# Kernel optimization log

Hardware: AMD Instinct MI355X
Metric: run time of the kernel (lower is better)

Reference implementation:

```python
import jax, jax.numpy as jnp
import numpy as np

B, CIN, COUT, N, K = 8, 128, 128, 2000, 16
IN_EPS = 1e-3   # InstanceNorm2d eps in module
BN_EPS = 1e-5   # BatchNorm2d default eps


def conv1x1(x, w, b):
    # x: [B,C,H,W], w: [O,C], b: [O]
    return jnp.einsum('bchw,oc->bohw', x, w) + b[None, :, None, None]


def setup_inputs() -> dict:
    key = jax.random.key(0)
    ks = jax.random.split(key, 12)
    s = 0.05
    return {
        'x_row':   jax.random.normal(ks[0], (B, COUT, N, 1), jnp.float32),
        'x_local': jax.random.normal(ks[1], (B, CIN, N, K), jnp.float32),
        'w0': jax.random.normal(ks[2], (COUT, CIN), jnp.float32) * s,
        'b0': jax.random.normal(ks[3], (COUT,), jnp.float32) * s,
        'bn_g': jnp.ones((COUT,), jnp.float32),
        'bn_b': jnp.zeros((COUT,), jnp.float32),
        'wq': jax.random.normal(ks[4], (COUT, COUT), jnp.float32) * s,
        'bq': jax.random.normal(ks[5], (COUT,), jnp.float32) * s,
        'wk': jax.random.normal(ks[6], (COUT, COUT), jnp.float32) * s,
        'bk': jax.random.normal(ks[7], (COUT,), jnp.float32) * s,
        'wv': jax.random.normal(ks[8], (COUT, COUT), jnp.float32) * s,
        'bv': jax.random.normal(ks[9], (COUT,), jnp.float32) * s,
        'gamma1': jnp.ones((1,), jnp.float32),
    }


def reference(x_row, x_local, w0, b0, bn_g, bn_b, wq, bq, wk, bk, wv, bv, gamma1):
    # att1: Conv1x1 -> InstanceNorm2d(eps=1e-3, no affine) -> BatchNorm2d (train-mode batch stats) -> ReLU
    h = conv1x1(x_local, w0, b0)                       # [B,C,N,K]
    mu = jnp.mean(h, axis=(2, 3), keepdims=True)
    var = jnp.var(h, axis=(2, 3), keepdims=True)
    h = (h - mu) * jax.lax.rsqrt(var + IN_EPS)
    bmu = jnp.mean(h, axis=(0, 2, 3), keepdims=True)
    bvar = jnp.var(h, axis=(0, 2, 3), keepdims=True)
    h = (h - bmu) * jax.lax.rsqrt(bvar + BN_EPS)
    h = h * bn_g[None, :, None, None] + bn_b[None, :, None, None]
    h = jax.nn.relu(h)

    q = conv1x1(h, wq, bq)
    k = conv1x1(h, wk, bk)
    v = conv1x1(h, wv, bv)
    att = jax.nn.softmax(q * k, axis=3)                # softmax over neighbor axis
    out_local = jnp.sum(att * v, axis=3, keepdims=True)  # [B,C,N,1]
    return x_row + gamma1 * out_local
```

## Files before the change

kernel.cpp:

```cpp
#include <hip/hip_runtime.h>
#include <math.h>

#define NB 8
#define NC 128
#define NPOS 2000
#define NK 32000
#define IN_EPS 1e-3f
#define BN_EPS 1e-5f

typedef short bf16x8 __attribute__((ext_vector_type(8)));
typedef float f32x4 __attribute__((ext_vector_type(4)));
typedef unsigned short ushort_t;

#define XSTRIDE 136

__device__ __forceinline__ f32x4 mfma_bf16(bf16x8 a, bf16x8 b, f32x4 c) {
  return __builtin_amdgcn_mfma_f32_16x16x32_bf16(a, b, c, 0, 0, 0);
}

__device__ __forceinline__ ushort_t f2bf(float f) {
  unsigned u = __float_as_uint(f);
  return (ushort_t)((u + 0x7FFFu + ((u >> 16) & 1u)) >> 16);
}


__global__ __launch_bounds__(256) void k_prep(const float* __restrict__ w0,
    const float* __restrict__ wq, const float* __restrict__ wk,
    const float* __restrict__ wv, ushort_t* __restrict__ wb) {
  int idx = blockIdx.x * 256 + threadIdx.x;
  int m = idx >> 14;
  int e = idx & 16383;
  const float* src = (m == 0) ? w0 : (m == 1) ? wq : (m == 2) ? wk : wv;
  wb[m * 16384 + e] = f2bf(src[e]);
}

__device__ __forceinline__ void stage_xt(const float* __restrict__ xb,
                                         ushort_t* __restrict__ xt, int tid) {
  const int col = tid & 127;
  const int hi = tid >> 7;
  const float* p = xb + col;
#pragma unroll
  for (int i = 0; i < 8; ++i) {
    const int c0 = hi * 64 + i * 8;
    ushort_t u[8] __attribute__((aligned(16)));
#pragma unroll
    for (int j = 0; j < 8; ++j) u[j] = f2bf(p[(size_t)(c0 + j) * NK]);
    *(uint4*)(xt + col * XSTRIDE + c0) = *(const uint4*)u;
  }
}

__global__ __launch_bounds__(256, 4) void k_stats(const float* __restrict__ x,
    const ushort_t* __restrict__ w0b, float* __restrict__ sum,
    float* __restrict__ sq) {
  __shared__ ushort_t xt[128 * XSTRIDE];
  const int b = blockIdx.y;
  const int col0 = blockIdx.x * 128;
  const int tid = threadIdx.x;
  stage_xt(x + (size_t)b * NC * NK + col0, xt, tid);
  __syncthreads();
  const int lane = tid & 63, w = tid >> 6;
  const int m = lane & 15, quad = lane >> 4;

#pragma unroll 1
  for (int p = 0; p < 2; ++p) {
    const int ch0 = (w + p * 4) * 16;
    bf16x8 wf[4];
#pragma unroll
    for (int kb = 0; kb < 4; ++kb)
      wf[kb] = *(const bf16x8*)(w0b + (ch0 + m) * 128 + kb * 32 + quad * 8);
    float s = 0.f, q2 = 0.f;
#pragma unroll 2
    for (int t = 0; t < 8; ++t) {
      const ushort_t* xr = xt + (t * 16 + m) * XSTRIDE;
      f32x4 acc = {0.f, 0.f, 0.f, 0.f};
#pragma unroll
      for (int kb = 0; kb < 4; ++kb) {
        bf16x8 af = *(const bf16x8*)(xr + kb * 32 + quad * 8);
        acc = mfma_bf16(af, wf[kb], acc);
      }
      s += (acc[0] + acc[1]) + (acc[2] + acc[3]);
      q2 += (acc[0] * acc[0] + acc[1] * acc[1]) +
            (acc[2] * acc[2] + acc[3] * acc[3]);
    }
    s += __shfl_xor(s, 16);
    s += __shfl_xor(s, 32);
    q2 += __shfl_xor(q2, 16);
    q2 += __shfl_xor(q2, 32);
    if (quad == 0) {
      atomicAdd(&sum[b * 128 + ch0 + m], s);
      atomicAdd(&sq[b * 128 + ch0 + m], q2);
    }
  }
}

__global__ void k_fold(const float* __restrict__ ws_in, const float* __restrict__ bn_g,
                       const float* __restrict__ bn_b, float* __restrict__ alpha,
                       float* __restrict__ beta) {
  int c = threadIdx.x;
  const float* sum = ws_in;
  const float* sq = ws_in + 1024;
  float var[NB], muv[NB];
  float bvar = 0.f;
#pragma unroll
  for (int b = 0; b < NB; ++b) {
    float mu = sum[b * 128 + c] * (1.f / NK);
    float v = sq[b * 128 + c] * (1.f / NK) - mu * mu;
    muv[b] = mu;
    var[b] = v;
    bvar += v / (v + IN_EPS);
  }
  bvar *= 0.125f;
  float s2 = rsqrtf(bvar + BN_EPS);
  float g = bn_g[c], bb = bn_b[c];
#pragma unroll
  for (int b = 0; b < NB; ++b) {
    float a = rsqrtf(var[b] + IN_EPS) * s2 * g;
    alpha[b * 128 + c] = a;
    beta[b * 128 + c] = bb - muv[b] * a;
  }
}

__global__ __launch_bounds__(256, 4) void k_fused(const float* __restrict__ x,
    const float* __restrict__ x_row, const ushort_t* __restrict__ wb,
    const float* __restrict__ alpha, const float* __restrict__ beta,
    const float* __restrict__ bq, const float* __restrict__ bk,
    const float* __restrict__ bv, const float* __restrict__ g1p,
    float* __restrict__ out) {
  __shared__ ushort_t xt[128 * XSTRIDE];
  __shared__ float souts[128 * 8];
  const int b = blockIdx.y;
  const int tid = threadIdx.x;
  stage_xt(x + (size_t)b * NC * NK + (size_t)blockIdx.x * 128, xt, tid);
  __syncthreads();
  const int lane = tid & 63, w = tid >> 6;
  const int m = lane & 15, quad = lane >> 4;
  const ushort_t* w0b = wb;
  const ushort_t* wqb = wb + 16384;
  const ushort_t* wkb = wb + 32768;
  const ushort_t* wvb = wb + 49152;

  uint2 hpk[2][8];
#pragma unroll
  for (int p = 0; p < 2; ++p) {
    const int ch0 = (w + p * 4) * 16;
    bf16x8 wf[4];
#pragma unroll
    for (int kb = 0; kb < 4; ++kb)
      wf[kb] = *(const bf16x8*)(w0b + (ch0 + m) * 128 + kb * 32 + quad * 8);
    const float4 av = *(const float4*)(alpha + b * 128 + ch0 + quad * 4);
    const float4 bev = *(const float4*)(beta + b * 128 + ch0 + quad * 4);
#pragma unroll
    for (int t = 0; t < 8; ++t) {
      const ushort_t* xr = xt + (t * 16 + m) * XSTRIDE;
      f32x4 acc = {0.f, 0.f, 0.f, 0.f};
#pragma unroll
      for (int kb = 0; kb < 4; ++kb) {
        bf16x8 bx = *(const bf16x8*)(xr + kb * 32 + quad * 8);
        acc = mfma_bf16(wf[kb], bx, acc);
      }
      float h0 = fmaxf(acc[0] * av.x + bev.x, 0.f);
      float h1 = fmaxf(acc[1] * av.y + bev.y, 0.f);
      float h2 = fmaxf(acc[2] * av.z + bev.z, 0.f);
      float h3 = fmaxf(acc[3] * av.w + bev.w, 0.f);
      uint2 pk;
      pk.x = (unsigned)f2bf(h0) | ((unsigned)f2bf(h1) << 16);
      pk.y = (unsigned)f2bf(h2) | ((unsigned)f2bf(h3) << 16);
      hpk[p][t] = pk;
    }
  }
  __syncthreads();
#pragma unroll
  for (int p = 0; p < 2; ++p)
#pragma unroll
    for (int t = 0; t < 8; ++t)
      *(uint2*)(xt + (t * 16 + m) * XSTRIDE + (w + p * 4) * 16 + quad * 4) =
          hpk[p][t];
  __syncthreads();

#pragma unroll 1
  for (int p = 0; p < 2; ++p) {
    const int ch0 = (w + p * 4) * 16;
    bf16x8 wqf[4], wkf[4], wvf[4];
#pragma unroll
    for (int kb = 0; kb < 4; ++kb) {
      wqf[kb] = *(const bf16x8*)(wqb + (ch0 + m) * 128 + kb * 32 + quad * 8);
      wkf[kb] = *(const bf16x8*)(wkb + (ch0 + m) * 128 + kb * 32 + quad * 8);
      wvf[kb] = *(const bf16x8*)(wvb + (ch0 + m) * 128 + kb * 32 + quad * 8);
    }
    const float bqv = bq[ch0 + m];
    const float bkv = bk[ch0 + m];
    const float bvv = bv[ch0 + m];
#pragma unroll 1
    for (int t = 0; t < 8; ++t) {
      const ushort_t* hr = xt + (t * 16 + m) * XSTRIDE;
      bf16x8 af[4];
#pragma unroll
      for (int kb = 0; kb < 4; ++kb)
        af[kb] = *(const bf16x8*)(hr + kb * 32 + quad * 8);
      f32x4 qa = {0.f, 0.f, 0.f, 0.f};
      f32x4 ka = {0.f, 0.f, 0.f, 0.f};
#pragma unroll
      for (int kb = 0; kb < 4; ++kb) qa = mfma_bf16(af[kb], wqf[kb], qa);
#pragma unroll
      for (int kb = 0; kb < 4; ++kb) ka = mfma_bf16(af[kb], wkf[kb], ka);
      float p0 = (qa[0] + bqv) * (ka[0] + bkv);
      float p1 = (qa[1] + bqv) * (ka[1] + bkv);
      float p2 = (qa[2] + bqv) * (ka[2] + bkv);
      float p3 = (qa[3] + bqv) * (ka[3] + bkv);
      float mx = fmaxf(fmaxf(p0, p1), fmaxf(p2, p3));
      mx = fmaxf(mx, __shfl_xor(mx, 16));
      mx = fmaxf(mx, __shfl_xor(mx, 32));
      float e0 = __expf(p0 - mx), e1 = __expf(p1 - mx);
      float e2 = __expf(p2 - mx), e3 = __expf(p3 - mx);
      float sm = (e0 + e1) + (e2 + e3);
      sm += __shfl_xor(sm, 16);
      sm += __shfl_xor(sm, 32);
      f32x4 va = {0.f, 0.f, 0.f, 0.f};
#pragma unroll
      for (int kb = 0; kb < 4; ++kb) va = mfma_bf16(af[kb], wvf[kb], va);
      float r0 = e0 * (va[0] + bvv) + e1 * (va[1] + bvv) +
                 e2 * (va[2] + bvv) + e3 * (va[3] + bvv);
      r0 += __shfl_xor(r0, 16);
      r0 += __shfl_xor(r0, 32);
      if (quad == 0) souts[(ch0 + m) * 8 + t] = r0 / sm;
    }
  }
  __syncthreads();

  {
    const float g1 = g1p[0];
    const int c = tid >> 1, half = tid & 1;
    const int n0 = blockIdx.x * 8 + half * 4;
    const size_t oi = ((size_t)b * NC + c) * NPOS + n0;
    const float4 xr = *(const float4*)(x_row + oi);
    const float* sp = souts + c * 8 + half * 4;
    float4 o;
    o.x = xr.x + g1 * sp[0];
    o.y = xr.y + g1 * sp[1];
    o.z = xr.z + g1 * sp[2];
    o.w = xr.w + g1 * sp[3];
    *(float4*)(out + oi) = o;
  }
}

extern "C" void kernel_launch(void* const* d_in, const int* in_sizes, int n_in,
                              void* d_out, int out_size, void* d_ws, size_t ws_size,
                              hipStream_t stream) {
  (void)in_sizes; (void)n_in; (void)out_size; (void)ws_size;
  const float* x_row   = (const float*)d_in[0];
  const float* x_local = (const float*)d_in[1];
  const float* w0   = (const float*)d_in[2];
  const float* bn_g = (const float*)d_in[4];
  const float* bn_b = (const float*)d_in[5];
  const float* wq   = (const float*)d_in[6];
  const float* bq   = (const float*)d_in[7];
  const float* wk   = (const float*)d_in[8];
  const float* bk   = (const float*)d_in[9];
  const float* wv   = (const float*)d_in[10];
  const float* bv   = (const float*)d_in[11];
  const float* gamma1 = (const float*)d_in[12];
  float* out = (float*)d_out;
  float* ws = (float*)d_ws;
  ushort_t* wb = (ushort_t*)((char*)d_ws + 16384);

  hipMemsetAsync(ws, 0, 2048 * sizeof(float), stream);
  k_prep<<<256, 256, 0, stream>>>(w0, wq, wk, wv, wb);
  k_stats<<<dim3(250, NB), 256, 0, stream>>>(x_local, wb, ws, ws + 1024);
  k_fold<<<1, 128, 0, stream>>>(ws, bn_g, bn_b, ws + 2048, ws + 3072);
  k_fused<<<dim3(250, NB), 256, 0, stream>>>(x_local, x_row, wb, ws + 2048,
                                             ws + 3072, bq, bk, bv, gamma1, out);
}
```

Baseline: 317.6 us.

## Halve fused-kernel tile to 64 columns and bucket stats atomics

The fused kernel now processes 64 columns (4 positions) per block across twice as many blocks. It uses a separate LDS buffer for the normalized activations, so the register staging and the extra barrier before the write-back go away. The stats kernel first reduces per-channel sums in shared memory, then spreads its global atomics over 32 buckets to cut contention, and k_fold sums the buckets. The trade-offs are a larger memset, more blocks each reloading weights, and half the threads idle in the output stage.

```diff
diff --git a/kernel.cpp b/kernel.cpp
--- a/kernel.cpp
+++ b/kernel.cpp
@@ -14,6 +14,12 @@
 
 #define XSTRIDE 136
 
+#define WSF_SUMP  0
+#define WSF_SQP   32768
+#define WSF_ALPHA 65536
+#define WSF_BETA  66560
+#define WSB_WEIGHTS 270336
+
 __device__ __forceinline__ f32x4 mfma_bf16(bf16x8 a, bf16x8 b, f32x4 c) {
   return __builtin_amdgcn_mfma_f32_16x16x32_bf16(a, b, c, 0, 0, 0);
 }
@@ -22,7 +28,6 @@
   unsigned u = __float_as_uint(f);
   return (ushort_t)((u + 0x7FFFu + ((u >> 16) & 1u)) >> 16);
 }
-
 
 __global__ __launch_bounds__(256) void k_prep(const float* __restrict__ w0,
     const float* __restrict__ wq, const float* __restrict__ wk,
@@ -34,8 +39,8 @@
   wb[m * 16384 + e] = f2bf(src[e]);
 }
 
-__device__ __forceinline__ void stage_xt(const float* __restrict__ xb,
-                                         ushort_t* __restrict__ xt, int tid) {
+__device__ __forceinline__ void stage_xt128(const float* __restrict__ xb,
+                                            ushort_t* __restrict__ xt, int tid) {
   const int col = tid & 127;
   const int hi = tid >> 7;
   const float* p = xb + col;
@@ -49,14 +54,29 @@
   }
 }
 
+__device__ __forceinline__ void stage_xt64(const float* __restrict__ xb,
+                                           ushort_t* __restrict__ xt, int tid) {
+  const int col = tid & 63;
+  const int hi = tid >> 6;
+  const float* p = xb + col;
+#pragma unroll
+  for (int i = 0; i < 4; ++i) {
+    const int c0 = hi * 32 + i * 8;
+    ushort_t u[8] __attribute__((aligned(16)));
+#pragma unroll
+    for (int j = 0; j < 8; ++j) u[j] = f2bf(p[(size_t)(c0 + j) * NK]);
+    *(uint4*)(xt + col * XSTRIDE + c0) = *(const uint4*)u;
+  }
+}
+
 __global__ __launch_bounds__(256, 4) void k_stats(const float* __restrict__ x,
-    const ushort_t* __restrict__ w0b, float* __restrict__ sum,
-    float* __restrict__ sq) {
+    const ushort_t* __restrict__ w0b, float* __restrict__ sumP,
+    float* __restrict__ sqP) {
   __shared__ ushort_t xt[128 * XSTRIDE];
+  __shared__ float ssum[128], ssq[128];
   const int b = blockIdx.y;
-  const int col0 = blockIdx.x * 128;
   const int tid = threadIdx.x;
-  stage_xt(x + (size_t)b * NC * NK + col0, xt, tid);
+  stage_xt128(x + (size_t)b * NC * NK + (size_t)blockIdx.x * 128, xt, tid);
   __syncthreads();
   const int lane = tid & 63, w = tid >> 6;
   const int m = lane & 15, quad = lane >> 4;
@@ -87,9 +107,15 @@
     q2 += __shfl_xor(q2, 16);
     q2 += __shfl_xor(q2, 32);
     if (quad == 0) {
-      atomicAdd(&sum[b * 128 + ch0 + m], s);
-      atomicAdd(&sq[b * 128 + ch0 + m], q2);
-    }
+      ssum[ch0 + m] = s;
+      ssq[ch0 + m] = q2;
+    }
+  }
+  __syncthreads();
+  if (tid < 128) {
+    const int bucket = blockIdx.x & 31;
+    atomicAdd(&sumP[bucket * 1024 + b * 128 + tid], ssum[tid]);
+    atomicAdd(&sqP[bucket * 1024 + b * 128 + tid], ssq[tid]);
   }
 }
 
@@ -97,14 +123,20 @@
                        const float* __restrict__ bn_b, float* __restrict__ alpha,
                        float* __restrict__ beta) {
   int c = threadIdx.x;
-  const float* sum = ws_in;
-  const float* sq = ws_in + 1024;
+  const float* sumP = ws_in + WSF_SUMP;
+  const float* sqP = ws_in + WSF_SQP;
   float var[NB], muv[NB];
   float bvar = 0.f;
-#pragma unroll
+#pragma unroll 1
   for (int b = 0; b < NB; ++b) {
-    float mu = sum[b * 128 + c] * (1.f / NK);
-    float v = sq[b * 128 + c] * (1.f / NK) - mu * mu;
+    float s = 0.f, q = 0.f;
+#pragma unroll
+    for (int k = 0; k < 32; ++k) {
+      s += sumP[k * 1024 + b * 128 + c];
+      q += sqP[k * 1024 + b * 128 + c];
+    }
+    float mu = s * (1.f / NK);
+    float v = q * (1.f / NK) - mu * mu;
     muv[b] = mu;
     var[b] = v;
     bvar += v / (v + IN_EPS);
@@ -126,11 +158,13 @@
     const float* __restrict__ bq, const float* __restrict__ bk,
     const float* __restrict__ bv, const float* __restrict__ g1p,
     float* __restrict__ out) {
-  __shared__ ushort_t xt[128 * XSTRIDE];
-  __shared__ float souts[128 * 8];
+  __shared__ ushort_t xt[64 * XSTRIDE];
+  __shared__ ushort_t ht[64 * XSTRIDE];
+  __shared__ float souts[128 * 5];
   const int b = blockIdx.y;
   const int tid = threadIdx.x;
-  stage_xt(x + (size_t)b * NC * NK + (size_t)blockIdx.x * 128, xt, tid);
+  stage_xt64(x + (size_t)b * NC * NK + (size_t)blockIdx.x * 64, xt, tid);
+  const float g1 = g1p[0];
   __syncthreads();
   const int lane = tid & 63, w = tid >> 6;
   const int m = lane & 15, quad = lane >> 4;
@@ -139,8 +173,7 @@
   const ushort_t* wkb = wb + 32768;
   const ushort_t* wvb = wb + 49152;
 
-  uint2 hpk[2][8];
-#pragma unroll
+#pragma unroll 1
   for (int p = 0; p < 2; ++p) {
     const int ch0 = (w + p * 4) * 16;
     bf16x8 wf[4];
@@ -150,7 +183,7 @@
     const float4 av = *(const float4*)(alpha + b * 128 + ch0 + quad * 4);
     const float4 bev = *(const float4*)(beta + b * 128 + ch0 + quad * 4);
 #pragma unroll
-    for (int t = 0; t < 8; ++t) {
+    for (int t = 0; t < 4; ++t) {
       const ushort_t* xr = xt + (t * 16 + m) * XSTRIDE;
       f32x4 acc = {0.f, 0.f, 0.f, 0.f};
 #pragma unroll
@@ -165,16 +198,9 @@
       uint2 pk;
       pk.x = (unsigned)f2bf(h0) | ((unsigned)f2bf(h1) << 16);
       pk.y = (unsigned)f2bf(h2) | ((unsigned)f2bf(h3) << 16);
-      hpk[p][t] = pk;
-    }
-  }
-  __syncthreads();
-#pragma unroll
-  for (int p = 0; p < 2; ++p)
-#pragma unroll
-    for (int t = 0; t < 8; ++t)
-      *(uint2*)(xt + (t * 16 + m) * XSTRIDE + (w + p * 4) * 16 + quad * 4) =
-          hpk[p][t];
+      *(uint2*)(ht + (t * 16 + m) * XSTRIDE + ch0 + quad * 4) = pk;
+    }
+  }
   __syncthreads();
 
 #pragma unroll 1
@@ -191,8 +217,8 @@
     const float bkv = bk[ch0 + m];
     const float bvv = bv[ch0 + m];
 #pragma unroll 1
-    for (int t = 0; t < 8; ++t) {
-      const ushort_t* hr = xt + (t * 16 + m) * XSTRIDE;
+    for (int t = 0; t < 4; ++t) {
+      const ushort_t* hr = ht + (t * 16 + m) * XSTRIDE;
       bf16x8 af[4];
 #pragma unroll
       for (int kb = 0; kb < 4; ++kb)
@@ -222,18 +248,16 @@
                  e2 * (va[2] + bvv) + e3 * (va[3] + bvv);
       r0 += __shfl_xor(r0, 16);
       r0 += __shfl_xor(r0, 32);
-      if (quad == 0) souts[(ch0 + m) * 8 + t] = r0 / sm;
-    }
-  }
-  __syncthreads();
-
-  {
-    const float g1 = g1p[0];
-    const int c = tid >> 1, half = tid & 1;
-    const int n0 = blockIdx.x * 8 + half * 4;
-    const size_t oi = ((size_t)b * NC + c) * NPOS + n0;
+      if (quad == 0) souts[(ch0 + m) * 5 + t] = r0 / sm;
+    }
+  }
+  __syncthreads();
+
+  if (tid < 128) {
+    const int c = tid;
+    const size_t oi = ((size_t)b * NC + c) * NPOS + blockIdx.x * 4;
     const float4 xr = *(const float4*)(x_row + oi);
-    const float* sp = souts + c * 8 + half * 4;
+    const float* sp = souts + c * 5;
     float4 o;
     o.x = xr.x + g1 * sp[0];
     o.y = xr.y + g1 * sp[1];
@@ -261,12 +285,14 @@
   const float* gamma1 = (const float*)d_in[12];
   float* out = (float*)d_out;
   float* ws = (float*)d_ws;
-  ushort_t* wb = (ushort_t*)((char*)d_ws + 16384);
-
-  hipMemsetAsync(ws, 0, 2048 * sizeof(float), stream);
+  ushort_t* wb = (ushort_t*)((char*)d_ws + WSB_WEIGHTS);
+
+  hipMemsetAsync(ws, 0, 65536 * sizeof(float), stream);
   k_prep<<<256, 256, 0, stream>>>(w0, wq, wk, wv, wb);
-  k_stats<<<dim3(250, NB), 256, 0, stream>>>(x_local, wb, ws, ws + 1024);
-  k_fold<<<1, 128, 0, stream>>>(ws, bn_g, bn_b, ws + 2048, ws + 3072);
-  k_fused<<<dim3(250, NB), 256, 0, stream>>>(x_local, x_row, wb, ws + 2048,
-                                             ws + 3072, bq, bk, bv, gamma1, out);
-}
+  k_stats<<<dim3(250, NB), 256, 0, stream>>>(x_local, wb, ws + WSF_SUMP,
+                                             ws + WSF_SQP);
+  k_fold<<<1, 128, 0, stream>>>(ws, bn_g, bn_b, ws + WSF_ALPHA, ws + WSF_BETA);
+  k_fused<<<dim3(500, NB), 256, 0, stream>>>(x_local, x_row, wb, ws + WSF_ALPHA,
+                                             ws + WSF_BETA, bq, bk, bv, gamma1,
+                                             out);
+}
```

Result: faster. 310.9 us (-2.1%).
